# Kernel tuning notes

Hardware: AMD Instinct MI355X
Metric: run time of the kernel (lower is better)

The kernel has to match this reference:

```python
import jax, jax.numpy as jnp
import numpy as np
from jax import lax

HEADS = 8

# Haar-lifting 4x4 matrices from nlwt_init / inlwt_init
U1P1 = jnp.array([[-0.5, -0.5, -0.5, 0.5], [0.5, -0.5, 0.5, 0.5], [0.5, 0.5, -0.5, 0.5], [0.5, -0.5, -0.5, -0.5]], jnp.float32)
U2P2 = jnp.array([[-1., 1., 1., -1.], [-1., -1., -1., -1.], [-1., -1., 1., 1.], [1., -1., 1., -1.]], jnp.float32)
P2U2 = jnp.array([[-1., -1., -1., 1.], [1., -1., -1., -1.], [1., -1., 1., 1.], [-1., -1., 1., -1.]], jnp.float32)
P1U1 = jnp.array([[-0.125, 0.125, 0.125, 0.125], [-0.125, -0.125, 0.125, -0.125], [-0.125, 0.125, -0.125, -0.125], [0.125, 0.125, 0.125, -0.125]], jnp.float32)


def conv1x1(x, w):
    # w: [out_ch, in_ch]
    return jnp.einsum('oi,bihw->bohw', w, x)


def dwconv3(x, w):
    # depthwise 3x3, w: [C,1,3,3]
    return lax.conv_general_dilated(x, w, (1, 1), [(1, 1), (1, 1)],
                                    dimension_numbers=('NCHW', 'OIHW', 'NCHW'),
                                    feature_group_count=x.shape[1])


def layernorm_c(x, w, b):
    # WithBias LayerNorm over channel dim (to_3d normalizes last dim == c)
    mu = jnp.mean(x, axis=1, keepdims=True)
    var = jnp.var(x, axis=1, keepdims=True)
    return (x - mu) / jnp.sqrt(var + 1e-5) * w[None, :, None, None] + b[None, :, None, None]


def attention(x, temperature, qkv_w, qkv_dw_w, proj_w):
    b, c, h, w = x.shape
    qkv = dwconv3(conv1x1(x, qkv_w), qkv_dw_w)
    q, k, v = jnp.split(qkv, 3, axis=1)
    hd = lambda t: t.reshape(b, HEADS, c // HEADS, h * w)
    q, k, v = hd(q), hd(k), hd(v)
    q = q / jnp.maximum(jnp.linalg.norm(q, axis=-1, keepdims=True), 1e-12)
    k = k / jnp.maximum(jnp.linalg.norm(k, axis=-1, keepdims=True), 1e-12)
    attn = jax.nn.softmax(jnp.einsum('bhcn,bhdn->bhcd', q, k) * temperature, axis=-1)
    out = jnp.einsum('bhcd,bhdn->bhcn', attn, v).reshape(b, c, h, w)
    return conv1x1(out, proj_w)


def ffn(x, pin_w, dw_w, pout_w):
    y = dwconv3(conv1x1(x, pin_w), dw_w)
    y1, y2 = jnp.split(y, 2, axis=1)
    return conv1x1(jax.nn.gelu(y1, approximate=False) * y2, pout_w)


def tblock(x, ln1_w, ln1_b, temperature, qkv_w, qkv_dw_w, proj_w, ln2_w, ln2_b, pin_w, ffn_dw_w, pout_w):
    x = x + attention(layernorm_c(x, ln1_w, ln1_b), temperature, qkv_w, qkv_dw_w, proj_w)
    x = x + ffn(layernorm_c(x, ln2_w, ln2_b), pin_w, ffn_dw_w, pout_w)
    return x


def nlwt(x):
    # lifting wavelet decompose (nlwt_init), vectorized im2col via reshape
    b, c, h, w = x.shape
    h1, w1 = h // 2, w // 2
    col = x.reshape(b, c, h1, 2, w1, 2).transpose(0, 1, 3, 5, 2, 4).reshape(b, c, 4, h1 * w1)
    x1 = jnp.einsum('ij,bcjn->bcin', U1P1, col).reshape(b, c, 4, h1, w1)
    t1 = x1[:, :, 0]
    t2 = jnp.roll(x1[:, :, 1], -1, axis=2)
    t3 = jnp.roll(x1[:, :, 2], -1, axis=3)
    t4 = jnp.roll(x1[:, :, 3], (-1, -1), axis=(2, 3))
    x1 = jnp.stack([t1, t2, t3, t4], axis=2).reshape(b, c, 4, h1 * w1)
    x2 = jnp.einsum('ij,bcjn->bcin', U2P2, x1).reshape(b, c, 4, h1, w1)
    return x2[:, :, 0], x2[:, :, 1], x2[:, :, 2], x2[:, :, 3]


def inlwt(A, B, C, D):
    # lifting wavelet reconstruct (inlwt_init), vectorized col2im via reshape
    b, c, h1, w1 = A.shape
    Y1 = jnp.stack([A, B, C, D], axis=2).reshape(b, c, 4, h1 * w1)
    Y2 = jnp.einsum('ij,bcjn->bcin', P2U2, Y1).reshape(b, c, 4, h1, w1)
    t1 = Y2[:, :, 0]
    t2 = jnp.roll(Y2[:, :, 1], 1, axis=2)
    t3 = jnp.roll(Y2[:, :, 2], 1, axis=3)
    t4 = jnp.roll(Y2[:, :, 3], (1, 1), axis=(2, 3))
    Y2 = jnp.stack([t1, t2, t3, t4], axis=2).reshape(b, c, 4, h1 * w1)
    Y3 = jnp.einsum('ij,bcjn->bcin', P1U1, Y2).reshape(b, c, 2, 2, h1, w1)
    return Y3.transpose(0, 1, 4, 2, 5, 3).reshape(b, c, 2 * h1, 2 * w1)


def gfm(x1, x2, ca_w1, ca_w2, sa_w, sa_b):
    Cc = x1.shape[1]
    cat = jnp.concatenate([x1, x2], axis=1)  # [b, 2C, h, w]
    avg = jnp.mean(cat, axis=(2, 3), keepdims=True)
    mx = jnp.max(cat, axis=(2, 3), keepdims=True)
    mlp = lambda t: conv1x1(jax.nn.relu(conv1x1(t, ca_w1)), ca_w2)
    cw = jax.nn.sigmoid(mlp(avg) + mlp(mx))  # [b, 2C, 1, 1]
    cw = cw.reshape(-1, 2, Cc)[:, :, :, None, None]
    out = cw[:, 0] * x1 + cw[:, 1] * x2
    savg = jnp.mean(out, axis=1, keepdims=True)
    smax = jnp.max(out, axis=1, keepdims=True)
    sa = lax.conv_general_dilated(jnp.concatenate([savg, smax], axis=1), sa_w, (1, 1), [(3, 3), (3, 3)],
                                  dimension_numbers=('NCHW', 'OIHW', 'NCHW')) + sa_b[None, :, None, None]
    return jax.nn.sigmoid(sa) * out


def setup_inputs() -> dict:
    key = jax.random.key(0)
    ks = jax.random.split(key, 16)
    B, C, H, W = 2, 48, 256, 256
    hidden = int(C * 2.66)  # 127
    s = 0.05
    return {
        'x': jax.random.normal(ks[0], (B, C, H, W), jnp.float32),
        'ln1_w': jnp.ones((C,), jnp.float32),
        'ln1_b': jnp.zeros((C,), jnp.float32),
        'temperature': jnp.ones((HEADS, 1, 1), jnp.float32),
        'qkv_w': jax.random.normal(ks[1], (3 * C, C), jnp.float32) * s,
        'qkv_dw_w': jax.random.normal(ks[2], (3 * C, 1, 3, 3), jnp.float32) * s,
        'proj_w': jax.random.normal(ks[3], (C, C), jnp.float32) * s,
        'ln2_w': jnp.ones((C,), jnp.float32),
        'ln2_b': jnp.zeros((C,), jnp.float32),
        'pin_w': jax.random.normal(ks[4], (2 * hidden, C), jnp.float32) * s,
        'ffn_dw_w': jax.random.normal(ks[5], (2 * hidden, 1, 3, 3), jnp.float32) * s,
        'pout_w': jax.random.normal(ks[6], (C, hidden), jnp.float32) * s,
        'ca_w1': jax.random.normal(ks[7], (2 * C // 16, 2 * C), jnp.float32) * s,
        'ca_w2': jax.random.normal(ks[8], (2 * C, 2 * C // 16), jnp.float32) * s,
        'sa_w': jax.random.normal(ks[9], (1, 2, 7, 7), jnp.float32) * s,
        'sa_b': jnp.zeros((1,), jnp.float32),
    }


def reference(x, ln1_w, ln1_b, temperature, qkv_w, qkv_dw_w, proj_w, ln2_w, ln2_b, pin_w, ffn_dw_w, pout_w, ca_w1, ca_w2, sa_w, sa_b):
    tb = lambda t: tblock(t, ln1_w, ln1_b, temperature, qkv_w, qkv_dw_w, proj_w, ln2_w, ln2_b, pin_w, ffn_dw_w, pout_w)
    branch1 = tb(x)
    A, Bh, Ch, Dh = nlwt(x)
    branch2 = inlwt(tb(A), Bh, Ch, Dh)
    return gfm(branch1, branch2, ca_w1, ca_w2, sa_w, sa_b)
```

## Files before the change

### kernel.cpp

```cpp
#include <hip/hip_runtime.h>
#include <math.h>

namespace {

constexpr int BB   = 2;
constexpr int CC   = 48;
constexpr int NHEAD= 8;
constexpr int CPH  = 6;
constexpr int HID  = 127;
constexpr int QKVC = 144;
constexpr int PINC = 254;
constexpr int N1   = 256*256;
constexpr int N2   = 128*128;
constexpr size_t PS2 = (size_t)BB*CC*N2;
constexpr size_t NB1 = (size_t)BB*CC*N1;

using short8  = __attribute__((ext_vector_type(8))) short;
using floatx4 = __attribute__((ext_vector_type(4))) float;

__device__ __forceinline__ float b2f(unsigned short u) {
    unsigned int x = ((unsigned int)u) << 16;
    float f; __builtin_memcpy(&f, &x, 4); return f;
}
__device__ __forceinline__ unsigned short f2b(float f) {
    unsigned int x; __builtin_memcpy(&x, &f, 4);
    unsigned int r = (x + 0x7FFFu + ((x >> 16) & 1u)) >> 16;
    return (unsigned short)r;
}
__device__ __forceinline__ unsigned int pack2(float lo, float hi) {
    return (unsigned int)f2b(lo) | ((unsigned int)f2b(hi) << 16);
}

__device__ __forceinline__ float gelu_t(float x) {
    float z = 1.5957691216057308f * (x + 0.044715f * x * x * x);
    float e = __expf(z);
    return x * (1.0f - 1.0f / (e + 1.0f));
}

__global__ void k_zero(float* __restrict__ p, int n)
{
    int i = blockIdx.x*256 + threadIdx.x;
    if (i < n) p[i] = 0.f;
}

__global__ void k_repw(const float* __restrict__ w, float* __restrict__ wt, int O, int K)
{
    int i = blockIdx.x*256 + threadIdx.x;
    if (i < O*K) {
        int c = i / O, oc = i - c*O;
        wt[c*O + oc] = w[oc*K + c];
    }
}

template<int OCR, int OCT>
__global__ void k_packw_mfma(const float* __restrict__ w, unsigned short* __restrict__ wf)
{
    int i = blockIdx.x*256 + threadIdx.x;
    if (i >= OCT*2*64) return;
    int lane = i & 63, ts = i >> 6;
    int s = ts & 1, t = ts >> 1;
    int oc = t*16 + (lane & 15);
    int kb = s*32 + (lane >> 4)*8;
    float v[8];
#pragma unroll
    for (int j = 0; j < 8; ++j) {
        int k = kb + j;
        v[j] = (oc < OCR && k < 48) ? w[oc*48 + k] : 0.f;
    }
    uint4 o;
    o.x = pack2(v[0], v[1]); o.y = pack2(v[2], v[3]);
    o.z = pack2(v[4], v[5]); o.w = pack2(v[6], v[7]);
    *(uint4*)(wf + (size_t)i*8) = o;
}

__global__ __launch_bounds__(256) void k_ln_t(const float* __restrict__ X,
                       const float* __restrict__ lw, const float* __restrict__ lb,
                       unsigned short* __restrict__ xh, int Ns)
{
    int g = blockIdx.x*256 + threadIdx.x;
    int half = Ns >> 1;
    int b = g / half, pp = (g - b*half)*2;
    const float* xb = X + (size_t)b*CC*Ns + pp;
    float v0[CC], v1[CC];
    float s0=0.f, s20=0.f, s1=0.f, s21=0.f;
#pragma unroll
    for (int c = 0; c < CC; ++c) {
        float2 v = *(const float2*)(xb + (size_t)c*Ns);
        v0[c]=v.x; v1[c]=v.y;
        s0 += v.x; s20 = fmaf(v.x,v.x,s20);
        s1 += v.y; s21 = fmaf(v.y,v.y,s21);
    }
    float mu0 = s0*(1.0f/CC), mu1 = s1*(1.0f/CC);
    float i0 = 1.0f/sqrtf(s20*(1.0f/CC)-mu0*mu0+1e-5f);
    float i1 = 1.0f/sqrtf(s21*(1.0f/CC)-mu1*mu1+1e-5f);
    unsigned short* r0 = xh + ((size_t)b*Ns + pp)*48;
    unsigned short* r1 = r0 + 48;
#pragma unroll
    for (int j = 0; j < 6; ++j) {
        uint4 o0, o1;
        float y[8], z[8];
#pragma unroll
        for (int e = 0; e < 8; ++e) {
            int c = j*8 + e;
            float w = lw[c], bb2 = lb[c];
            y[e] = (v0[c]-mu0)*i0*w + bb2;
            z[e] = (v1[c]-mu1)*i1*w + bb2;
        }
        o0.x = pack2(y[0],y[1]); o0.y = pack2(y[2],y[3]);
        o0.z = pack2(y[4],y[5]); o0.w = pack2(y[6],y[7]);
        o1.x = pack2(z[0],z[1]); o1.y = pack2(z[2],z[3]);
        o1.z = pack2(z[4],z[5]); o1.w = pack2(z[6],z[7]);
        *(uint4*)(r0 + j*8) = o0;
        *(uint4*)(r1 + j*8) = o1;
    }
}

template<int OCR, int OCT>
__global__ __launch_bounds__(256) void k_conv_mfma(const unsigned short* __restrict__ xh,
                       const unsigned short* __restrict__ wf,
                       unsigned short* __restrict__ out, int Ns)
{
    int wid = (blockIdx.x*256 + (int)threadIdx.x) >> 6;
    int lane = threadIdx.x & 63;
    int tpb = Ns >> 4;
    int b = wid / tpb, pxt = wid - b*tpb;
    int px0 = pxt << 4;
    int col = lane & 15, grp = lane >> 4;
    const unsigned short* xb = xh + ((size_t)b*Ns + px0 + col)*48 + grp*8;
    short8 b0 = *(const short8*)(xb);
    short8 b1 = *(const short8*)(xb + 32);
    unsigned short* ob = out + (size_t)b*OCR*Ns + px0 + col;
    int ocb0 = grp*4;
#pragma unroll
    for (int t = 0; t < OCT; ++t) {
        floatx4 acc = {};
        short8 a0 = *(const short8*)(wf + (size_t)((t*2+0)*64 + lane)*8);
        short8 a1 = *(const short8*)(wf + (size_t)((t*2+1)*64 + lane)*8);
        acc = __builtin_amdgcn_mfma_f32_16x16x32_bf16(a0, b0, acc, 0, 0, 0);
        acc = __builtin_amdgcn_mfma_f32_16x16x32_bf16(a1, b1, acc, 0, 0, 0);
#pragma unroll
        for (int r = 0; r < 4; ++r) {
            int oc = t*16 + ocb0 + r;
            if (OCR % 16 == 0 || oc < OCR)
                ob[(size_t)oc*Ns] = f2b(acc[r]);
        }
    }
}

__device__ __forceinline__ void load_row10(const unsigned short* __restrict__ p,
                                           bool rok, bool lok, bool rrok, float (&f)[10])
{
    if (rok) {
        uint4 cv = *(const uint4*)p;
        unsigned int u0=cv.x,u1=cv.y,u2=cv.z,u3=cv.w;
        f[1]=b2f((unsigned short)(u0&0xffffu)); f[2]=b2f((unsigned short)(u0>>16));
        f[3]=b2f((unsigned short)(u1&0xffffu)); f[4]=b2f((unsigned short)(u1>>16));
        f[5]=b2f((unsigned short)(u2&0xffffu)); f[6]=b2f((unsigned short)(u2>>16));
        f[7]=b2f((unsigned short)(u3&0xffffu)); f[8]=b2f((unsigned short)(u3>>16));
        f[0] = lok  ? b2f(p[-1]) : 0.f;
        f[9] = rrok ? b2f(p[8])  : 0.f;
    } else {
#pragma unroll
        for (int i = 0; i < 10; ++i) f[i] = 0.f;
    }
}

__device__ __forceinline__ void dw8(const unsigned short* __restrict__ plane,
                                    const float* __restrict__ w9,
                                    int y, int x0, int Hs, int Ws, float (&o)[8])
{
#pragma unroll
    for (int i = 0; i < 8; ++i) o[i] = 0.f;
#pragma unroll
    for (int dy = 0; dy < 3; ++dy) {
        int r = y + dy - 1;
        bool rok = (r >= 0) && (r < Hs);
        float f[10];
        const unsigned short* p = plane + (size_t)(rok ? r : 0)*Ws + x0;
        load_row10(p, rok, x0 > 0, x0 + 8 < Ws, f);
        float w0 = w9[dy*3], w1 = w9[dy*3+1], w2 = w9[dy*3+2];
#pragma unroll
        for (int i = 0; i < 8; ++i)
            o[i] = fmaf(f[i], w0, fmaf(f[i+1], w1, fmaf(f[i+2], w2, o[i])));
    }
}

__global__ __launch_bounds__(256) void k_dw3v(const unsigned short* __restrict__ in,
                      const float* __restrict__ w,
                      float* __restrict__ out, int nch, int Hs, int Ws)
{
    int Ns = Hs * Ws, ng = Ns >> 3, wq = Ws >> 3;
    int g = blockIdx.x*256 + threadIdx.x;
    int t = g % ng, bc = g / ng;
    int c = bc % nch;
    int y = t / wq, x0 = (t - y*wq) << 3;
    float o[8];
    dw8(in + (size_t)bc*Ns, w + c*9, y, x0, Hs, Ws, o);
    float4* ob = (float4*)(out + (size_t)bc*Ns + y*Ws + x0);
    ob[0] = make_float4(o[0],o[1],o[2],o[3]);
    ob[1] = make_float4(o[4],o[5],o[6],o[7]);
}

__global__ __launch_bounds__(256) void k_dwgate(const unsigned short* __restrict__ pin,
                         const float* __restrict__ dww,
                         unsigned short* __restrict__ gate, int Hs, int Ws)
{
    int Ns = Hs * Ws, ng = Ns >> 3, wq = Ws >> 3;
    int g = blockIdx.x*256 + threadIdx.x;
    int t = g % ng, bc = g / ng;
    int b = bc / HID, c = bc - b*HID;
    int y = t / wq, x0 = (t - y*wq) << 3;
    float d1[8], d2[8];
    dw8(pin + ((size_t)b*PINC + c)*Ns,       dww + c*9,         y, x0, Hs, Ws, d1);
    dw8(pin + ((size_t)b*PINC + HID + c)*Ns, dww + (c+HID)*9,   y, x0, Hs, Ws, d2);
    uint4 r;
    r.x = pack2(gelu_t(d1[0])*d2[0], gelu_t(d1[1])*d2[1]);
    r.y = pack2(gelu_t(d1[2])*d2[2], gelu_t(d1[3])*d2[3]);
    r.z = pack2(gelu_t(d1[4])*d2[4], gelu_t(d1[5])*d2[5]);
    r.w = pack2(gelu_t(d1[6])*d2[6], gelu_t(d1[7])*d2[7]);
    *(uint4*)(gate + (size_t)bc*Ns + y*Ws + x0) = r;
}

__global__ __launch_bounds__(256) void k_qk_stats(const float* __restrict__ qkvd,
                                                  float* __restrict__ st, int Ns)
{
    const int NBLK = 32;
    int bh = blockIdx.x / NBLK, blk = blockIdx.x % NBLK;
    int b = bh / NHEAD, h = bh % NHEAD;
    const float* qb = qkvd + ((size_t)b*QKVC + h*CPH)*Ns;
    const float* kb = qkvd + ((size_t)b*QKVC + 48 + h*CPH)*Ns;
    float vals[48];
#pragma unroll
    for (int i = 0; i < 48; ++i) vals[i] = 0.f;
    for (int n = blk*256 + (int)threadIdx.x; n < Ns; n += NBLK*256) {
        float qv[CPH], kv[CPH];
#pragma unroll
        for (int i = 0; i < CPH; ++i) { qv[i] = qb[(size_t)i*Ns + n]; kv[i] = kb[(size_t)i*Ns + n]; }
#pragma unroll
        for (int i = 0; i < CPH; ++i) {
            vals[i]   = fmaf(qv[i], qv[i], vals[i]);
            vals[6+i] = fmaf(kv[i], kv[i], vals[6+i]);
        }
#pragma unroll
        for (int i = 0; i < CPH; ++i)
#pragma unroll
            for (int j = 0; j < CPH; ++j)
                vals[12 + i*6 + j] = fmaf(qv[i], kv[j], vals[12 + i*6 + j]);
    }
    __shared__ float red[4][48];
    int lane = threadIdx.x & 63, wave = threadIdx.x >> 6;
#pragma unroll
    for (int i = 0; i < 48; ++i) {
        float v = vals[i];
#pragma unroll
        for (int off = 32; off > 0; off >>= 1) v += __shfl_down(v, off);
        if (lane == 0) red[wave][i] = v;
    }
    __syncthreads();
    if ((int)threadIdx.x < 48) {
        int i = threadIdx.x;
        float v = red[0][i] + red[1][i] + red[2][i] + red[3][i];
        float* dst;
        if (i < 6)       dst = st + b*48 + h*CPH + i;
        else if (i < 12) dst = st + 96 + b*48 + h*CPH + (i-6);
        else             dst = st + 192 + (b*NHEAD+h)*36 + (i-12);
        atomicAdd(dst, v);
    }
}

__global__ void k_attn(const float* __restrict__ st, const float* __restrict__ temp,
                       float* __restrict__ ao)
{
    int t = threadIdx.x;
    if (t >= BB*NHEAD) return;
    int b = t / NHEAD, h = t % NHEAD;
    const float* sqq = st + b*48 + h*CPH;
    const float* sqk = st + 96 + b*48 + h*CPH;
    const float* g   = st + 192 + (b*NHEAD+h)*36;
    float T = temp[h];
    float nq[CPH], nk[CPH];
#pragma unroll
    for (int i = 0; i < CPH; ++i) {
        nq[i] = fmaxf(sqrtf(sqq[i]), 1e-12f);
        nk[i] = fmaxf(sqrtf(sqk[i]), 1e-12f);
    }
    float* out = ao + (b*NHEAD+h)*36;
#pragma unroll
    for (int c = 0; c < CPH; ++c) {
        float l[CPH]; float m = -1e30f;
#pragma unroll
        for (int d = 0; d < CPH; ++d) {
            l[d] = g[c*6+d] / (nq[c]*nk[d]) * T;
            m = fmaxf(m, l[d]);
        }
        float ssum = 0.f;
#pragma unroll
        for (int d = 0; d < CPH; ++d) { l[d] = expf(l[d]-m); ssum += l[d]; }
        float r = 1.0f/ssum;
#pragma unroll
        for (int d = 0; d < CPH; ++d) out[c*6+d] = l[d]*r;
    }
}

__global__ __launch_bounds__(256) void k_av_proj(const float* __restrict__ qkvd, const float* __restrict__ attn,
                          const float* __restrict__ projw, const float* __restrict__ X,
                          float* __restrict__ x1, int Ns)
{
    int g = blockIdx.x*256 + threadIdx.x;
    int b = g / Ns, p = g - b*Ns;
    int ocb = blockIdx.y * 16;
    const float* vb = qkvd + ((size_t)b*QKVC + 96)*Ns + p;
    float vv[CC];
#pragma unroll
    for (int c = 0; c < CC; ++c) vv[c] = vb[(size_t)c*Ns];
    const float* at = attn + b*288;
    float o[CC];
#pragma unroll
    for (int h = 0; h < NHEAD; ++h)
#pragma unroll
        for (int cc = 0; cc < CPH; ++cc) {
            float acc = 0.f;
#pragma unroll
            for (int d = 0; d < CPH; ++d)
                acc = fmaf(at[(h*CPH+cc)*CPH + d], vv[h*CPH + d], acc);
            o[h*CPH+cc] = acc;
        }
    const float* xb = X + (size_t)b*CC*Ns + p;
    float* ob = x1 + (size_t)b*CC*Ns + p;
    float acc[16];
#pragma unroll
    for (int i = 0; i < 16; ++i) acc[i] = 0.f;
#pragma unroll
    for (int c = 0; c < CC; ++c) {
#pragma unroll
        for (int i = 0; i < 16; ++i)
            acc[i] = fmaf(o[c], projw[(ocb+i)*CC + c], acc[i]);
    }
#pragma unroll
    for (int i = 0; i < 16; ++i)
        ob[(size_t)(ocb+i)*Ns] = xb[(size_t)(ocb+i)*Ns] + acc[i];
}

template<int U>
__device__ __forceinline__ void pout_chunk(const unsigned short* __restrict__ gb, int c0, int Ns,
                                           const float* __restrict__ wt, int ocb,
                                           float (&a0)[16], float (&a1)[16])
{
    unsigned int gv[U];
#pragma unroll
    for (int u = 0; u < U; ++u)
        gv[u] = *(const unsigned int*)(gb + (size_t)(c0+u)*Ns);
#pragma unroll
    for (int u = 0; u < U; ++u) {
        float t0 = b2f((unsigned short)(gv[u] & 0xffffu));
        float t1 = b2f((unsigned short)(gv[u] >> 16));
        const float* wr = wt + (c0+u)*48 + ocb;
#pragma unroll
        for (int i = 0; i < 16; ++i) {
            float w = wr[i];
            a0[i] = fmaf(t0, w, a0[i]);
            a1[i] = fmaf(t1, w, a1[i]);
        }
    }
}

__global__ __launch_bounds__(256) void k_pout(const unsigned short* __restrict__ gate,
                       const float* __restrict__ wt, const float* __restrict__ x1,
                       float* __restrict__ out, int Ns)
{
    int g = blockIdx.x*256 + threadIdx.x;
    int half = Ns >> 1;
    int b = g / half, pp = (g - b*half)*2;
    int ocb = blockIdx.y * 16;
    const unsigned short* gb = gate + (size_t)b*HID*Ns + pp;
    float a0[16], a1[16];
#pragma unroll
    for (int i = 0; i < 16; ++i) { a0[i] = 0.f; a1[i] = 0.f; }
    int c = 0;
    for (; c + 8 <= HID; c += 8)
        pout_chunk<8>(gb, c, Ns, wt, ocb, a0, a1);
    pout_chunk<7>(gb, c, Ns, wt, ocb, a0, a1);
    const float* xb = x1 + (size_t)b*CC*Ns + pp;
    float* ob = out + (size_t)b*CC*Ns + pp;
#pragma unroll
    for (int i = 0; i < 16; ++i) {
        float2 xv = *(const float2*)(xb + (size_t)(ocb+i)*Ns);
        float2 o; o.x = xv.x + a0[i]; o.y = xv.y + a1[i];
        *(float2*)(ob + (size_t)(ocb+i)*Ns) = o;
    }
}

__global__ __launch_bounds__(256) void k_nlwt(const float* __restrict__ X, float* __restrict__ A4)
{
    int g = blockIdx.x*256 + threadIdx.x;
    int n = g & (N2-1); int bc = g >> 14;
    int h1 = n >> 7, w1 = n & 127;
    int hb = (h1+1)&127, wb = (w1+1)&127;
    const float* xp = X + (size_t)bc * N1;
    float t1, t2, t3, t4;
    {
        int y=h1, z=w1;
        float c0=xp[(2*y)*256+2*z], c1=xp[(2*y)*256+2*z+1], c2=xp[(2*y+1)*256+2*z], c3=xp[(2*y+1)*256+2*z+1];
        t1 = 0.5f*(-c0 - c1 - c2 + c3);
    }
    {
        int y=hb, z=w1;
        float c0=xp[(2*y)*256+2*z], c1=xp[(2*y)*256+2*z+1], c2=xp[(2*y+1)*256+2*z], c3=xp[(2*y+1)*256+2*z+1];
        t2 = 0.5f*( c0 - c1 + c2 + c3);
    }
    {
        int y=h1, z=wb;
        float c0=xp[(2*y)*256+2*z], c1=xp[(2*y)*256+2*z+1], c2=xp[(2*y+1)*256+2*z], c3=xp[(2*y+1)*256+2*z+1];
        t3 = 0.5f*( c0 + c1 - c2 + c3);
    }
    {
        int y=hb, z=wb;
        float c0=xp[(2*y)*256+2*z], c1=xp[(2*y)*256+2*z+1], c2=xp[(2*y+1)*256+2*z], c3=xp[(2*y+1)*256+2*z+1];
        t4 = 0.5f*( c0 - c1 - c2 - c3);
    }
    size_t o = (size_t)bc*N2 + n;
    A4[o]           = -t1 + t2 + t3 - t4;
    A4[PS2 + o]     = -t1 - t2 - t3 - t4;
    A4[2*PS2 + o]   = -t1 - t2 + t3 + t4;
    A4[3*PS2 + o]   =  t1 - t2 + t3 - t4;
}

__global__ __launch_bounds__(256) void k_inlwt(const float* __restrict__ Ain, const float* __restrict__ A4,
                        float* __restrict__ out)
{
    int g = blockIdx.x*256 + threadIdx.x;
    int n = g & (N2-1); int bc = g >> 14;
    int h1 = n >> 7, w1 = n & 127;
    int hm = (h1-1)&127, wm = (w1-1)&127;
    const float* I0 = Ain + (size_t)bc*N2;
    const float* I1 = A4 + PS2   + (size_t)bc*N2;
    const float* I2 = A4 + 2*PS2 + (size_t)bc*N2;
    const float* I3 = A4 + 3*PS2 + (size_t)bc*N2;
    int i00 = h1*128+w1, i10 = hm*128+w1, i01 = h1*128+wm, i11 = hm*128+wm;
    float t1, t2, t3, t4;
    { float a=I0[i00], b2=I1[i00], c2=I2[i00], d2=I3[i00]; t1 = -a - b2 - c2 + d2; }
    { float a=I0[i10], b2=I1[i10], c2=I2[i10], d2=I3[i10]; t2 =  a - b2 - c2 - d2; }
    { float a=I0[i01], b2=I1[i01], c2=I2[i01], d2=I3[i01]; t3 =  a - b2 + c2 + d2; }
    { float a=I0[i11], b2=I1[i11], c2=I2[i11], d2=I3[i11]; t4 = -a - b2 + c2 - d2; }
    float y00 = 0.125f*(-t1 + t2 + t3 + t4);
    float y01 = 0.125f*(-t1 - t2 + t3 - t4);
    float y10 = 0.125f*(-t1 + t2 - t3 - t4);
    float y11 = 0.125f*( t1 + t2 + t3 - t4);
    float* ob = out + (size_t)bc * N1;
    int oy = h1*2, ox = w1*2;
    ob[(size_t)oy*256 + ox]       = y00;
    ob[(size_t)oy*256 + ox + 1]   = y01;
    ob[(size_t)(oy+1)*256 + ox]   = y10;
    ob[(size_t)(oy+1)*256 + ox+1] = y11;
}

constexpr int CSEG = 8;
__global__ __launch_bounds__(256) void k_chstat_part(const float* __restrict__ b1, const float* __restrict__ b2,
                         float* __restrict__ ps, float* __restrict__ pm)
{
    int bc = blockIdx.x;
    int seg = blockIdx.y;
    int b = bc / 96, ch = bc % 96;
    const float* src = (ch < 48 ? b1 + ((size_t)b*CC + ch)*N1
                                : b2 + ((size_t)b*CC + (ch-48))*N1) + (size_t)seg*(N1/CSEG);
    const float4* s4 = (const float4*)src;
    float s = 0.f, m = -1e30f;
    for (int i = threadIdx.x; i < N1/CSEG/4; i += 256) {
        float4 v = s4[i];
        s += v.x+v.y+v.z+v.w;
        m = fmaxf(m, fmaxf(fmaxf(v.x,v.y), fmaxf(v.z,v.w)));
    }
    int lane = threadIdx.x & 63, wave = threadIdx.x >> 6;
    __shared__ float rs[4], rm[4];
#pragma unroll
    for (int off = 32; off > 0; off >>= 1) {
        s += __shfl_down(s, off);
        m = fmaxf(m, __shfl_down(m, off));
    }
    if (lane == 0) { rs[wave] = s; rm[wave] = m; }
    __syncthreads();
    if (threadIdx.x == 0) {
        ps[bc*CSEG + seg] = rs[0]+rs[1]+rs[2]+rs[3];
        pm[bc*CSEG + seg] = fmaxf(fmaxf(rm[0],rm[1]), fmaxf(rm[2],rm[3]));
    }
}

__global__ void k_chstat_fin(const float* __restrict__ ps, const float* __restrict__ pm,
                             float* __restrict__ avg, float* __restrict__ mxo)
{
    int t = threadIdx.x;
    if (t >= BB*96) return;
    float s = 0.f, m = -1e30f;
#pragma unroll
    for (int j = 0; j < CSEG; ++j) {
        s += ps[t*CSEG+j];
        m = fmaxf(m, pm[t*CSEG+j]);
    }
    avg[t] = s*(1.0f/N1);
    mxo[t] = m;
}

__global__ void k_cw(const float* __restrict__ avg, const float* __restrict__ mx,
                     const float* __restrict__ w1, const float* __restrict__ w2,
                     float* __restrict__ cw)
{
    int t = threadIdx.x;
    if (t >= BB*96) return;
    int b = t / 96, o = t % 96;
    float ta[6], tm[6];
#pragma unroll
    for (int j = 0; j < 6; ++j) {
        float sa = 0.f, sm = 0.f;
        for (int i = 0; i < 96; ++i) {
            float w = w1[j*96+i];
            sa = fmaf(w, avg[b*96+i], sa);
            sm = fmaf(w, mx[b*96+i], sm);
        }
        ta[j] = sa > 0.f ? sa : 0.f;
        tm[j] = sm > 0.f ? sm : 0.f;
    }
    float ua = 0.f, um = 0.f;
#pragma unroll
    for (int j = 0; j < 6; ++j) {
        ua = fmaf(w2[o*6+j], ta[j], ua);
        um = fmaf(w2[o*6+j], tm[j], um);
    }
    float z = ua + um;
    cw[t] = 1.0f/(1.0f+expf(-z));
}

__global__ __launch_bounds__(256) void k_gfm_out(const float* __restrict__ b1, const float* __restrict__ b2,
                          const float* __restrict__ cw, float* __restrict__ ob,
                          float* __restrict__ savg, float* __restrict__ smax)
{
    int g = blockIdx.x*256 + threadIdx.x;
    int b = g >> 16, p = g & (N1-1);
    float s = 0.f, m = -1e30f;
#pragma unroll
    for (int c = 0; c < CC; ++c) {
        size_t idx = ((size_t)b*CC + c)*N1 + p;
        float o = cw[b*96 + c]*b1[idx] + cw[b*96 + 48 + c]*b2[idx];
        ob[idx] = o;
        s += o; m = fmaxf(m, o);
    }
    savg[(size_t)b*N1 + p] = s*(1.0f/CC);
    smax[(size_t)b*N1 + p] = m;
}

__global__ __launch_bounds__(256) void k_final(const float* __restrict__ savg, const float* __restrict__ smax,
                        const float* __restrict__ saw, const float* __restrict__ sab,
                        const float* __restrict__ ob, float* __restrict__ out)
{
    int g = blockIdx.x*256 + threadIdx.x;
    int b = g >> 16, p = g & (N1-1);
    int y = p >> 8, x = p & 255;
    float s = sab[0];
    const float* av = savg + (size_t)b*N1;
    const float* mx = smax + (size_t)b*N1;
#pragma unroll
    for (int ky = 0; ky < 7; ++ky) {
        int yy = y + ky - 3;
        bool yok = (yy >= 0) && (yy < 256);
        int yc = yy < 0 ? 0 : (yy > 255 ? 255 : yy);
#pragma unroll
        for (int kx = 0; kx < 7; ++kx) {
            int xx = x + kx - 3;
            bool ok = yok && (xx >= 0) && (xx < 256);
            int xc = xx < 0 ? 0 : (xx > 255 ? 255 : xx);
            int idx = yc*256 + xc;
            float a = av[idx], m2 = mx[idx];
            s = fmaf(ok ? a  : 0.f, saw[ky*7+kx], s);
            s = fmaf(ok ? m2 : 0.f, saw[49 + ky*7+kx], s);
        }
    }
    float sig = 1.0f/(1.0f+expf(-s));
#pragma unroll
    for (int c = 0; c < CC; ++c) {
        size_t idx = ((size_t)b*CC + c)*N1 + p;
        out[idx] = sig * ob[idx];
    }
}

}

extern "C" void kernel_launch(void* const* d_in, const int* in_sizes, int n_in,
                              void* d_out, int out_size, void* d_ws, size_t ws_size,
                              hipStream_t stream)
{
    const float* x    = (const float*)d_in[0];
    const float* ln1w = (const float*)d_in[1];
    const float* ln1b = (const float*)d_in[2];
    const float* temp = (const float*)d_in[3];
    const float* qkvw = (const float*)d_in[4];
    const float* qkvdw= (const float*)d_in[5];
    const float* projw= (const float*)d_in[6];
    const float* ln2w = (const float*)d_in[7];
    const float* ln2b = (const float*)d_in[8];
    const float* pinw = (const float*)d_in[9];
    const float* ffdw = (const float*)d_in[10];
    const float* poutw= (const float*)d_in[11];
    const float* caw1 = (const float*)d_in[12];
    const float* caw2 = (const float*)d_in[13];
    const float* saw  = (const float*)d_in[14];
    const float* sab  = (const float*)d_in[15];

    float* wsf  = (float*)d_ws;
    float* A4   = wsf;
    float* br1  = A4 + 4*PS2;
    float* br2  = br1 + NB1;
    float* x1b  = br2 + NB1;
    float* tbA  = x1b + NB1;
    float* qkv  = tbA + PS2;
    float* qkvd = qkv + (size_t)BB*QKVC*N1;
    float* stats= qkvd + (size_t)BB*QKVC*N1;
    float* wfqf = stats + 4096;
    float* wfpf = wfqf + 4608;
    float* wor  = wfpf + 8192;
    float* chps = wor + HID*48;
    float* chpm = chps + 192*CSEG;
    float* savg = chpm + 192*CSEG;
    float* smax = savg + (size_t)BB*N1;

    unsigned short* wfq = (unsigned short*)wfqf;
    unsigned short* wfp = (unsigned short*)wfpf;

    k_packw_mfma<QKVC, 9><<<(9*2*64+255)/256, 256, 0, stream>>>(qkvw, wfq);
    k_packw_mfma<PINC, 16><<<(16*2*64+255)/256, 256, 0, stream>>>(pinw, wfp);
    k_repw<<<(HID*48+255)/256, 256, 0, stream>>>(poutw, wor, 48, HID);

    auto tb = [&](const float* Xin, float* outp, int Hs, int Ws) {
        int Ns = Hs*Ws;
        int npix = BB*Ns;
        unsigned short* xhat = (unsigned short*)qkvd;
        k_zero<<<3, 256, 0, stream>>>(stats, 768);
        k_ln_t<<<npix/512, 256, 0, stream>>>(Xin, ln1w, ln1b, xhat, Ns);
        k_conv_mfma<QKVC, 9><<<npix/64, 256, 0, stream>>>(xhat, wfq, (unsigned short*)qkv, Ns);
        k_dw3v<<<(BB*QKVC*Ns/8)/256, 256, 0, stream>>>((const unsigned short*)qkv, qkvdw, qkvd, QKVC, Hs, Ws);
        k_qk_stats<<<BB*NHEAD*32, 256, 0, stream>>>(qkvd, stats, Ns);
        k_attn<<<1, 64, 0, stream>>>(stats, temp, stats + 768);
        dim3 g4(npix/256, 3);
        k_av_proj<<<g4, 256, 0, stream>>>(qkvd, stats + 768, projw, Xin, x1b, Ns);
        k_ln_t<<<npix/512, 256, 0, stream>>>(x1b, ln2w, ln2b, xhat, Ns);
        k_conv_mfma<PINC, 16><<<npix/64, 256, 0, stream>>>(xhat, wfp, (unsigned short*)qkv, Ns);
        k_dwgate<<<(BB*HID*Ns/8)/256, 256, 0, stream>>>((const unsigned short*)qkv, ffdw,
                                                        (unsigned short*)qkvd, Hs, Ws);
        dim3 g6(npix/512, 3);
        k_pout<<<g6, 256, 0, stream>>>((const unsigned short*)qkvd, wor, x1b, outp, Ns);
    };

    tb(x, br1, 256, 256);
    k_nlwt<<<(BB*CC*N2)/256, 256, 0, stream>>>(x, A4);
    tb(A4, tbA, 128, 128);
    k_inlwt<<<(BB*CC*N2)/256, 256, 0, stream>>>(tbA, A4, br2);
    dim3 gc(BB*96, CSEG);
    k_chstat_part<<<gc, 256, 0, stream>>>(br1, br2, chps, chpm);
    k_chstat_fin<<<1, 256, 0, stream>>>(chps, chpm, stats + 1344, stats + 1536);
    k_cw<<<1, 256, 0, stream>>>(stats + 1344, stats + 1536, caw1, caw2, stats + 1728);
    k_gfm_out<<<(BB*N1)/256, 256, 0, stream>>>(br1, br2, stats + 1728, x1b, savg, smax);
    k_final<<<(BB*N1)/256, 256, 0, stream>>>(savg, smax, saw, sab, x1b, (float*)d_out);
}
```

Measured before the change: 430.2 us.

## Store depthwise qkv in bf16, tile dwconv 4 rows, fold proj into attention

The depthwise conv kernels now compute a 4x8 output tile per thread, so each loaded input row serves up to three output rows. The qkv depthwise output is stored as bf16 instead of fp32, which halves the traffic written by k_dw3v and read by k_qk_stats and k_av_proj. The per-head attention matrix is folded into the projection weights inside k_attn as a 48x48 matrix per batch, and k_av_proj does one matmul over two pixels per thread. Integer divides are replaced by shifts and compares. The cost is lower precision in q/k/v and serial matrix folding in a single-thread-per-head kernel.

After: 437.2 us. No clear change (+1.6%).

```diff
diff --git a/kernel.cpp b/kernel.cpp
--- a/kernel.cpp
+++ b/kernel.cpp
@@ -79,7 +79,8 @@
 {
     int g = blockIdx.x*256 + threadIdx.x;
     int half = Ns >> 1;
-    int b = g / half, pp = (g - b*half)*2;
+    int b = g >= half ? 1 : 0;
+    int pp = (g - b*half)*2;
     const float* xb = X + (size_t)b*CC*Ns + pp;
     float v0[CC], v1[CC];
     float s0=0.f, s20=0.f, s1=0.f, s21=0.f;
@@ -148,104 +149,120 @@
 }
 
 __device__ __forceinline__ void load_row10(const unsigned short* __restrict__ p,
-                                           bool rok, bool lok, bool rrok, float (&f)[10])
-{
-    if (rok) {
-        uint4 cv = *(const uint4*)p;
-        unsigned int u0=cv.x,u1=cv.y,u2=cv.z,u3=cv.w;
-        f[1]=b2f((unsigned short)(u0&0xffffu)); f[2]=b2f((unsigned short)(u0>>16));
-        f[3]=b2f((unsigned short)(u1&0xffffu)); f[4]=b2f((unsigned short)(u1>>16));
-        f[5]=b2f((unsigned short)(u2&0xffffu)); f[6]=b2f((unsigned short)(u2>>16));
-        f[7]=b2f((unsigned short)(u3&0xffffu)); f[8]=b2f((unsigned short)(u3>>16));
-        f[0] = lok  ? b2f(p[-1]) : 0.f;
-        f[9] = rrok ? b2f(p[8])  : 0.f;
-    } else {
-#pragma unroll
-        for (int i = 0; i < 10; ++i) f[i] = 0.f;
-    }
-}
-
-__device__ __forceinline__ void dw8(const unsigned short* __restrict__ plane,
-                                    const float* __restrict__ w9,
-                                    int y, int x0, int Hs, int Ws, float (&o)[8])
-{
-#pragma unroll
-    for (int i = 0; i < 8; ++i) o[i] = 0.f;
-#pragma unroll
-    for (int dy = 0; dy < 3; ++dy) {
-        int r = y + dy - 1;
-        bool rok = (r >= 0) && (r < Hs);
+                                           bool lok, bool rrok, float (&f)[10])
+{
+    uint4 cv = *(const uint4*)p;
+    unsigned int u0=cv.x,u1=cv.y,u2=cv.z,u3=cv.w;
+    f[1]=b2f((unsigned short)(u0&0xffffu)); f[2]=b2f((unsigned short)(u0>>16));
+    f[3]=b2f((unsigned short)(u1&0xffffu)); f[4]=b2f((unsigned short)(u1>>16));
+    f[5]=b2f((unsigned short)(u2&0xffffu)); f[6]=b2f((unsigned short)(u2>>16));
+    f[7]=b2f((unsigned short)(u3&0xffffu)); f[8]=b2f((unsigned short)(u3>>16));
+    f[0] = lok  ? b2f(p[-1]) : 0.f;
+    f[9] = rrok ? b2f(p[8])  : 0.f;
+}
+
+__device__ __forceinline__ void dw4x8(const unsigned short* __restrict__ plane,
+                                      const float* __restrict__ w9,
+                                      int y0, int x0, int Hs, int Ws, float (&acc)[4][8])
+{
+#pragma unroll
+    for (int r = 0; r < 4; ++r)
+#pragma unroll
+        for (int i = 0; i < 8; ++i) acc[r][i] = 0.f;
+    bool lok = x0 > 0, rrok = x0 + 8 < Ws;
+#pragma unroll
+    for (int ir = 0; ir < 6; ++ir) {
+        int r = y0 + ir - 1;
+        if (r < 0 || r >= Hs) continue;
         float f[10];
-        const unsigned short* p = plane + (size_t)(rok ? r : 0)*Ws + x0;
-        load_row10(p, rok, x0 > 0, x0 + 8 < Ws, f);
-        float w0 = w9[dy*3], w1 = w9[dy*3+1], w2 = w9[dy*3+2];
-#pragma unroll
-        for (int i = 0; i < 8; ++i)
-            o[i] = fmaf(f[i], w0, fmaf(f[i+1], w1, fmaf(f[i+2], w2, o[i])));
+        load_row10(plane + (size_t)r*Ws + x0, lok, rrok, f);
+#pragma unroll
+        for (int ky = 0; ky < 3; ++ky) {
+            int orow = ir - ky;
+            if (orow < 0 || orow > 3) continue;
+            float w0 = w9[ky*3], w1 = w9[ky*3+1], w2 = w9[ky*3+2];
+#pragma unroll
+            for (int i = 0; i < 8; ++i)
+                acc[orow][i] = fmaf(f[i], w0, fmaf(f[i+1], w1, fmaf(f[i+2], w2, acc[orow][i])));
+        }
     }
 }
 
 __global__ __launch_bounds__(256) void k_dw3v(const unsigned short* __restrict__ in,
                       const float* __restrict__ w,
-                      float* __restrict__ out, int nch, int Hs, int Ws)
-{
-    int Ns = Hs * Ws, ng = Ns >> 3, wq = Ws >> 3;
-    int g = blockIdx.x*256 + threadIdx.x;
-    int t = g % ng, bc = g / ng;
-    int c = bc % nch;
-    int y = t / wq, x0 = (t - y*wq) << 3;
-    float o[8];
-    dw8(in + (size_t)bc*Ns, w + c*9, y, x0, Hs, Ws, o);
-    float4* ob = (float4*)(out + (size_t)bc*Ns + y*Ws + x0);
-    ob[0] = make_float4(o[0],o[1],o[2],o[3]);
-    ob[1] = make_float4(o[4],o[5],o[6],o[7]);
+                      unsigned short* __restrict__ out, int Hs, int Ws, int lgNgt, int lgWq)
+{
+    int g = blockIdx.x*256 + threadIdx.x;
+    int t = g & ((1<<lgNgt)-1), bc = g >> lgNgt;
+    int c = bc % QKVC;
+    int y0 = (t >> lgWq) << 2, x0 = (t & ((1<<lgWq)-1)) << 3;
+    int Ns = Hs*Ws;
+    float acc[4][8];
+    dw4x8(in + (size_t)bc*Ns, w + c*9, y0, x0, Hs, Ws, acc);
+    unsigned short* ob = out + (size_t)bc*Ns + (size_t)y0*Ws + x0;
+#pragma unroll
+    for (int r = 0; r < 4; ++r) {
+        uint4 o;
+        o.x = pack2(acc[r][0],acc[r][1]); o.y = pack2(acc[r][2],acc[r][3]);
+        o.z = pack2(acc[r][4],acc[r][5]); o.w = pack2(acc[r][6],acc[r][7]);
+        *(uint4*)(ob + (size_t)r*Ws) = o;
+    }
 }
 
 __global__ __launch_bounds__(256) void k_dwgate(const unsigned short* __restrict__ pin,
                          const float* __restrict__ dww,
-                         unsigned short* __restrict__ gate, int Hs, int Ws)
-{
-    int Ns = Hs * Ws, ng = Ns >> 3, wq = Ws >> 3;
-    int g = blockIdx.x*256 + threadIdx.x;
-    int t = g % ng, bc = g / ng;
+                         unsigned short* __restrict__ gate, int Hs, int Ws, int lgNgt, int lgWq)
+{
+    int g = blockIdx.x*256 + threadIdx.x;
+    int t = g & ((1<<lgNgt)-1), bc = g >> lgNgt;
     int b = bc / HID, c = bc - b*HID;
-    int y = t / wq, x0 = (t - y*wq) << 3;
-    float d1[8], d2[8];
-    dw8(pin + ((size_t)b*PINC + c)*Ns,       dww + c*9,         y, x0, Hs, Ws, d1);
-    dw8(pin + ((size_t)b*PINC + HID + c)*Ns, dww + (c+HID)*9,   y, x0, Hs, Ws, d2);
-    uint4 r;
-    r.x = pack2(gelu_t(d1[0])*d2[0], gelu_t(d1[1])*d2[1]);
-    r.y = pack2(gelu_t(d1[2])*d2[2], gelu_t(d1[3])*d2[3]);
-    r.z = pack2(gelu_t(d1[4])*d2[4], gelu_t(d1[5])*d2[5]);
-    r.w = pack2(gelu_t(d1[6])*d2[6], gelu_t(d1[7])*d2[7]);
-    *(uint4*)(gate + (size_t)bc*Ns + y*Ws + x0) = r;
-}
-
-__global__ __launch_bounds__(256) void k_qk_stats(const float* __restrict__ qkvd,
+    int y0 = (t >> lgWq) << 2, x0 = (t & ((1<<lgWq)-1)) << 3;
+    int Ns = Hs*Ws;
+    float a1[4][8], a2[4][8];
+    dw4x8(pin + ((size_t)b*PINC + c)*Ns,       dww + c*9,       y0, x0, Hs, Ws, a1);
+    dw4x8(pin + ((size_t)b*PINC + HID + c)*Ns, dww + (c+HID)*9, y0, x0, Hs, Ws, a2);
+    unsigned short* ob = gate + (size_t)bc*Ns + (size_t)y0*Ws + x0;
+#pragma unroll
+    for (int r = 0; r < 4; ++r) {
+        uint4 o;
+        o.x = pack2(gelu_t(a1[r][0])*a2[r][0], gelu_t(a1[r][1])*a2[r][1]);
+        o.y = pack2(gelu_t(a1[r][2])*a2[r][2], gelu_t(a1[r][3])*a2[r][3]);
+        o.z = pack2(gelu_t(a1[r][4])*a2[r][4], gelu_t(a1[r][5])*a2[r][5]);
+        o.w = pack2(gelu_t(a1[r][6])*a2[r][6], gelu_t(a1[r][7])*a2[r][7]);
+        *(uint4*)(ob + (size_t)r*Ws) = o;
+    }
+}
+
+__global__ __launch_bounds__(256) void k_qk_stats(const unsigned short* __restrict__ qkvd,
                                                   float* __restrict__ st, int Ns)
 {
     const int NBLK = 32;
     int bh = blockIdx.x / NBLK, blk = blockIdx.x % NBLK;
     int b = bh / NHEAD, h = bh % NHEAD;
-    const float* qb = qkvd + ((size_t)b*QKVC + h*CPH)*Ns;
-    const float* kb = qkvd + ((size_t)b*QKVC + 48 + h*CPH)*Ns;
+    const unsigned short* qb = qkvd + ((size_t)b*QKVC + h*CPH)*Ns;
+    const unsigned short* kb = qkvd + ((size_t)b*QKVC + 48 + h*CPH)*Ns;
     float vals[48];
 #pragma unroll
     for (int i = 0; i < 48; ++i) vals[i] = 0.f;
-    for (int n = blk*256 + (int)threadIdx.x; n < Ns; n += NBLK*256) {
-        float qv[CPH], kv[CPH];
-#pragma unroll
-        for (int i = 0; i < CPH; ++i) { qv[i] = qb[(size_t)i*Ns + n]; kv[i] = kb[(size_t)i*Ns + n]; }
+    for (int n = blk*512 + (int)threadIdx.x*2; n < Ns; n += NBLK*512) {
+        float q0[CPH], q1[CPH], k0[CPH], k1[CPH];
 #pragma unroll
         for (int i = 0; i < CPH; ++i) {
-            vals[i]   = fmaf(qv[i], qv[i], vals[i]);
-            vals[6+i] = fmaf(kv[i], kv[i], vals[6+i]);
+            unsigned int qu = *(const unsigned int*)(qb + (size_t)i*Ns + n);
+            unsigned int ku = *(const unsigned int*)(kb + (size_t)i*Ns + n);
+            q0[i] = b2f((unsigned short)(qu & 0xffffu)); q1[i] = b2f((unsigned short)(qu >> 16));
+            k0[i] = b2f((unsigned short)(ku & 0xffffu)); k1[i] = b2f((unsigned short)(ku >> 16));
+        }
+#pragma unroll
+        for (int i = 0; i < CPH; ++i) {
+            vals[i]   = fmaf(q0[i],q0[i], fmaf(q1[i],q1[i], vals[i]));
+            vals[6+i] = fmaf(k0[i],k0[i], fmaf(k1[i],k1[i], vals[6+i]));
         }
 #pragma unroll
         for (int i = 0; i < CPH; ++i)
 #pragma unroll
             for (int j = 0; j < CPH; ++j)
-                vals[12 + i*6 + j] = fmaf(qv[i], kv[j], vals[12 + i*6 + j]);
+                vals[12+i*6+j] = fmaf(q0[i],k0[j], fmaf(q1[i],k1[j], vals[12+i*6+j]));
     }
     __shared__ float red[4][48];
     int lane = threadIdx.x & 63, wave = threadIdx.x >> 6;
@@ -269,7 +286,7 @@
 }
 
 __global__ void k_attn(const float* __restrict__ st, const float* __restrict__ temp,
-                       float* __restrict__ ao)
+                       const float* __restrict__ projw, float* __restrict__ Mt)
 {
     int t = threadIdx.x;
     if (t >= BB*NHEAD) return;
@@ -284,7 +301,7 @@
         nq[i] = fmaxf(sqrtf(sqq[i]), 1e-12f);
         nk[i] = fmaxf(sqrtf(sqk[i]), 1e-12f);
     }
-    float* out = ao + (b*NHEAD+h)*36;
+    float a[CPH][CPH];
 #pragma unroll
     for (int c = 0; c < CPH; ++c) {
         float l[CPH]; float m = -1e30f;
@@ -298,47 +315,62 @@
         for (int d = 0; d < CPH; ++d) { l[d] = expf(l[d]-m); ssum += l[d]; }
         float r = 1.0f/ssum;
 #pragma unroll
-        for (int d = 0; d < CPH; ++d) out[c*6+d] = l[d]*r;
-    }
-}
-
-__global__ __launch_bounds__(256) void k_av_proj(const float* __restrict__ qkvd, const float* __restrict__ attn,
-                          const float* __restrict__ projw, const float* __restrict__ X,
+        for (int d = 0; d < CPH; ++d) a[c][d] = l[d]*r;
+    }
+    float* mb = Mt + b*CC*CC;
+#pragma unroll
+    for (int d = 0; d < CPH; ++d) {
+        for (int oc = 0; oc < CC; ++oc) {
+            float m = 0.f;
+#pragma unroll
+            for (int c = 0; c < CPH; ++c)
+                m = fmaf(projw[oc*CC + h*CPH + c], a[c][d], m);
+            mb[(h*CPH+d)*CC + oc] = m;
+        }
+    }
+}
+
+__global__ __launch_bounds__(256) void k_av_proj(const unsigned short* __restrict__ qkvd,
+                          const float* __restrict__ Mt, const float* __restrict__ X,
                           float* __restrict__ x1, int Ns)
 {
     int g = blockIdx.x*256 + threadIdx.x;
-    int b = g / Ns, p = g - b*Ns;
+    int half = Ns >> 1;
+    int b = g >= half ? 1 : 0;
+    int pp = (g - b*half)*2;
     int ocb = blockIdx.y * 16;
-    const float* vb = qkvd + ((size_t)b*QKVC + 96)*Ns + p;
-    float vv[CC];
-#pragma unroll
-    for (int c = 0; c < CC; ++c) vv[c] = vb[(size_t)c*Ns];
-    const float* at = attn + b*288;
-    float o[CC];
-#pragma unroll
-    for (int h = 0; h < NHEAD; ++h)
-#pragma unroll
-        for (int cc = 0; cc < CPH; ++cc) {
-            float acc = 0.f;
-#pragma unroll
-            for (int d = 0; d < CPH; ++d)
-                acc = fmaf(at[(h*CPH+cc)*CPH + d], vv[h*CPH + d], acc);
-            o[h*CPH+cc] = acc;
-        }
-    const float* xb = X + (size_t)b*CC*Ns + p;
-    float* ob = x1 + (size_t)b*CC*Ns + p;
-    float acc[16];
-#pragma unroll
-    for (int i = 0; i < 16; ++i) acc[i] = 0.f;
-#pragma unroll
-    for (int c = 0; c < CC; ++c) {
-#pragma unroll
-        for (int i = 0; i < 16; ++i)
-            acc[i] = fmaf(o[c], projw[(ocb+i)*CC + c], acc[i]);
-    }
-#pragma unroll
-    for (int i = 0; i < 16; ++i)
-        ob[(size_t)(ocb+i)*Ns] = xb[(size_t)(ocb+i)*Ns] + acc[i];
+    const unsigned short* vb = qkvd + ((size_t)b*QKVC + 96)*Ns + pp;
+    const float* mt = Mt + b*CC*CC;
+    float a0[16], a1[16];
+#pragma unroll
+    for (int i = 0; i < 16; ++i) { a0[i] = 0.f; a1[i] = 0.f; }
+#pragma unroll
+    for (int c0 = 0; c0 < CC; c0 += 8) {
+        unsigned int gv[8];
+#pragma unroll
+        for (int u = 0; u < 8; ++u)
+            gv[u] = *(const unsigned int*)(vb + (size_t)(c0+u)*Ns);
+#pragma unroll
+        for (int u = 0; u < 8; ++u) {
+            float t0 = b2f((unsigned short)(gv[u] & 0xffffu));
+            float t1 = b2f((unsigned short)(gv[u] >> 16));
+            const float* wr = mt + (c0+u)*CC + ocb;
+#pragma unroll
+            for (int i = 0; i < 16; ++i) {
+                float w = wr[i];
+                a0[i] = fmaf(t0, w, a0[i]);
+                a1[i] = fmaf(t1, w, a1[i]);
+            }
+        }
+    }
+    const float* xb = X + (size_t)b*CC*Ns + pp;
+    float* ob = x1 + (size_t)b*CC*Ns + pp;
+#pragma unroll
+    for (int i = 0; i < 16; ++i) {
+        float2 xv = *(const float2*)(xb + (size_t)(ocb+i)*Ns);
+        float2 o; o.x = xv.x + a0[i]; o.y = xv.y + a1[i];
+        *(float2*)(ob + (size_t)(ocb+i)*Ns) = o;
+    }
 }
 
 template<int U>
@@ -370,7 +402,8 @@
 {
     int g = blockIdx.x*256 + threadIdx.x;
     int half = Ns >> 1;
-    int b = g / half, pp = (g - b*half)*2;
+    int b = g >= half ? 1 : 0;
+    int pp = (g - b*half)*2;
     int ocb = blockIdx.y * 16;
     const unsigned short* gb = gate + (size_t)b*HID*Ns + pp;
     float a0[16], a1[16];
@@ -581,6 +614,8 @@
     }
 }
 
+__device__ __forceinline__ int ilog2(int v) { return 31 - __builtin_clz(v); }
+
 }
 
 extern "C" void kernel_launch(void* const* d_in, const int* in_sizes, int n_in,
@@ -620,6 +655,7 @@
     float* chpm = chps + 192*CSEG;
     float* savg = chpm + 192*CSEG;
     float* smax = savg + (size_t)BB*N1;
+    float* Mt   = smax + (size_t)BB*N1;
 
     unsigned short* wfq = (unsigned short*)wfqf;
     unsigned short* wfp = (unsigned short*)wfpf;
@@ -631,19 +667,22 @@
     auto tb = [&](const float* Xin, float* outp, int Hs, int Ws) {
         int Ns = Hs*Ws;
         int npix = BB*Ns;
+        int lgWq = 31 - __builtin_clz(Ws >> 3);
+        int lgNgt = (31 - __builtin_clz(Hs >> 2)) + lgWq;
         unsigned short* xhat = (unsigned short*)qkvd;
         k_zero<<<3, 256, 0, stream>>>(stats, 768);
         k_ln_t<<<npix/512, 256, 0, stream>>>(Xin, ln1w, ln1b, xhat, Ns);
         k_conv_mfma<QKVC, 9><<<npix/64, 256, 0, stream>>>(xhat, wfq, (unsigned short*)qkv, Ns);
-        k_dw3v<<<(BB*QKVC*Ns/8)/256, 256, 0, stream>>>((const unsigned short*)qkv, qkvdw, qkvd, QKVC, Hs, Ws);
-        k_qk_stats<<<BB*NHEAD*32, 256, 0, stream>>>(qkvd, stats, Ns);
-        k_attn<<<1, 64, 0, stream>>>(stats, temp, stats + 768);
-        dim3 g4(npix/256, 3);
-        k_av_proj<<<g4, 256, 0, stream>>>(qkvd, stats + 768, projw, Xin, x1b, Ns);
+        k_dw3v<<<(BB*QKVC*(Ns/32))/256, 256, 0, stream>>>((const unsigned short*)qkv, qkvdw,
+                                                          (unsigned short*)qkvd, Hs, Ws, lgNgt, lgWq);
+        k_qk_stats<<<BB*NHEAD*32, 256, 0, stream>>>((const unsigned short*)qkvd, stats, Ns);
+        k_attn<<<1, 64, 0, stream>>>(stats, temp, projw, Mt);
+        dim3 g4(npix/512, 3);
+        k_av_proj<<<g4, 256, 0, stream>>>((const unsigned short*)qkvd, Mt, Xin, x1b, Ns);
         k_ln_t<<<npix/512, 256, 0, stream>>>(x1b, ln2w, ln2b, xhat, Ns);
         k_conv_mfma<PINC, 16><<<npix/64, 256, 0, stream>>>(xhat, wfp, (unsigned short*)qkv, Ns);
-        k_dwgate<<<(BB*HID*Ns/8)/256, 256, 0, stream>>>((const unsigned short*)qkv, ffdw,
-                                                        (unsigned short*)qkvd, Hs, Ws);
+        k_dwgate<<<(BB*HID*(Ns/32)+255)/256, 256, 0, stream>>>((const unsigned short*)qkv, ffdw,
+                                                        (unsigned short*)qkvd, Hs, Ws, lgNgt, lgWq);
         dim3 g6(npix/512, 3);
         k_pout<<<g6, 256, 0, stream>>>((const unsigned short*)qkvd, wor, x1b, outp, Ns);
     };
```
